# Kernel optimization log

Measured on AMD Instinct MI355X. Metric: run time of the kernel, lower is better.

The kernel has to match this reference:

```python
import jax, jax.numpy as jnp
import numpy as np

# Workspace layout (static slice bounds, per init_kwargs)
SS, SE = 0, 512        # spoke
HPS, HPE = 512, 768    # hub private
HSS, HSE = 768, 1024   # hub shared
TS, TE = 1024, 1088    # tag
HS, HE = 512, 1024     # full hub (priv + shared) for the read path

B, T, D_STATE, D_MODEL, D_LATENT = 8, 4096, 1088, 1024, 128


def setup_inputs() -> dict:
    key = jax.random.key(0)
    ks = jax.random.split(key, 10)
    scale = 0.02  # typical init scale for learned projections
    return {
        "S": jax.random.normal(ks[0], (B, T, D_STATE), jnp.float32),
        "w_spoke": jax.random.normal(ks[1], (B, T, SE - SS), jnp.float32),
        "w_hub_priv": jax.random.normal(ks[2], (B, T, HPE - HPS), jnp.float32),
        "w_hub_shared": jax.random.normal(ks[3], (B, T, HSE - HSS), jnp.float32),
        "tag": jax.random.normal(ks[4], (B, T, TE - TS), jnp.float32),
        "W_read": jax.random.normal(ks[5], (D_MODEL, D_STATE), jnp.float32) * scale,
        "cache": jnp.zeros((B, T, D_LATENT), jnp.float32),
        "latent": jax.random.normal(ks[6], (B, T, D_LATENT), jnp.float32),
        "Wk": jax.random.normal(ks[7], (D_MODEL, D_LATENT), jnp.float32) * scale,
        "Wv": jax.random.normal(ks[8], (D_MODEL, D_LATENT), jnp.float32) * scale,
    }


def reference(S, w_spoke, w_hub_priv, w_hub_shared, tag, W_read, cache, latent, Wk, Wv):
    # --- fused_workspace_write: four independent slice-adds into S ---
    S = S.at[:, :, SS:SE].add(w_spoke)
    S = S.at[:, :, HPS:HPE].add(w_hub_priv)
    S = S.at[:, :, HSS:HSE].add(w_hub_shared)
    S = S.at[:, :, TS:TE].add(tag)

    # --- fused_workspace_read: concat(spoke, hub, tag) then F.linear(., W_read) ---
    readable = jnp.concatenate(
        [S[:, :, SS:SE], S[:, :, HS:HE], S[:, :, TS:TE]], axis=-1
    )  # (B, T, D_STATE)
    out = jnp.einsum("btr,dr->btd", readable, W_read)  # (B, T, D_MODEL)

    # --- CWTLatentCache.update: overwrite latents at start_position=0 ---
    cache = jax.lax.dynamic_update_slice(cache, latent, (0, 0, 0))

    # --- K/V reconstruction from compressed latents via up-projections ---
    k = jnp.einsum("btl,dl->btd", cache, Wk)  # (B, T, D_MODEL)
    v = jnp.einsum("btl,dl->btd", cache, Wv)  # (B, T, D_MODEL)
    return (out, k, v)
```

## Files before the change

kernel.cpp:

```cpp
#include <hip/hip_runtime.h>

typedef __attribute__((ext_vector_type(8))) _Float16 half8;
typedef __attribute__((ext_vector_type(2))) __fp16 half2r;
typedef __attribute__((ext_vector_type(4))) float f32x4;

#define AS1 __attribute__((address_space(1)))
#define AS3 __attribute__((address_space(3)))

union H2U { half2r h; unsigned int u; };
union Frag { half8 v; unsigned long long d[2]; };

__device__ __forceinline__ unsigned int pk(float a, float b) {
    H2U x; x.h = __builtin_amdgcn_cvt_pkrtz(a, b); return x.u;
}

__device__ __forceinline__ void gload_lds16(const void* g, void* l) {
    __builtin_amdgcn_global_load_lds((const AS1 unsigned int*)g,
                                     (AS3 unsigned int*)l, 16, 0, 0);
}

#define W1_ROWB 2176
#define WS2_OFF 2228224
#define W2_ROWB 256
#define A_ROWB  2176

__device__ __forceinline__ void pick_w(int ks, const float* wsp, const float* whp,
                                       const float* whs, const float* wtg,
                                       const float*& wbase, int& wstr, int& wko) {
    if (ks < 8)       { wbase = wsp; wstr = 512; wko = ks * 64; }
    else if (ks < 12) { wbase = whp; wstr = 256; wko = ks * 64 - 512; }
    else if (ks < 16) { wbase = whs; wstr = 256; wko = ks * 64 - 768; }
    else              { wbase = wtg; wstr = 64;  wko = 0; }
}

__global__ __launch_bounds__(256) void prep_w(const float* __restrict__ Wr,
                                              const float* __restrict__ Wk,
                                              const float* __restrict__ Wv,
                                              char* __restrict__ ws) {
    int id = blockIdx.x * 256 + threadIdx.x;
    if (id < 272 * 1024) {
        int n = id / 272;
        int k = (id % 272) * 4;
        f32x4 w = *(const f32x4*)(Wr + (size_t)n * 1088 + k);
        uint2 q; q.x = pk(w.x, w.y); q.y = pk(w.z, w.w);
        size_t off = (size_t)n * W1_ROWB + ((k >> 6) << 7)
                   + (((k & 63) << 1) ^ ((n & 7) << 4));
        *(uint2*)(ws + off) = q;
    } else {
        int j = id - 272 * 1024;
        int r = j >> 5;
        int k = (j & 31) << 2;
        const float* src = (r < 1024) ? (Wk + (size_t)r * 128 + k)
                                      : (Wv + (size_t)(r - 1024) * 128 + k);
        f32x4 w = *(const f32x4*)src;
        uint2 q; q.x = pk(w.x, w.y); q.y = pk(w.z, w.w);
        size_t off = WS2_OFF + (size_t)r * W2_ROWB + ((k >> 6) << 7)
                   + (((k & 63) << 1) ^ ((r & 7) << 4));
        *(uint2*)(ws + off) = q;
    }
}

__global__ __launch_bounds__(256)
void fuse_a(const float* __restrict__ S, const float* __restrict__ wsp,
            const float* __restrict__ whp, const float* __restrict__ whs,
            const float* __restrict__ wtg, char* __restrict__ a16) {
    int u = blockIdx.x * 256 + threadIdx.x;
    int row = u / 272;
    int rem = u % 272;
    int ks = rem >> 4;
    int k4 = (rem & 15) << 2;

    const float* wbase; int wstr, wko;
    pick_w(ks, wsp, whp, whs, wtg, wbase, wstr, wko);

    f32x4 s4 = *(const f32x4*)(S + (size_t)row * 1088 + ks * 64 + k4);
    f32x4 w4 = *(const f32x4*)(wbase + (size_t)row * wstr + wko + k4);
    uint2 q; q.x = pk(s4.x + w4.x, s4.y + w4.y);
             q.y = pk(s4.z + w4.z, s4.w + w4.w);
    size_t off = (size_t)row * A_ROWB + (ks << 7)
               + (((k4) << 1) ^ ((row & 7) << 4));
    *(uint2*)(a16 + off) = q;
}

__global__ __launch_bounds__(256, 2)
void gemm_read(const char* __restrict__ wsA, const char* __restrict__ wws,
               float* __restrict__ out) {
    __shared__ char lds[65536];

    int bid = blockIdx.x;
    int wg   = (bid & 7) * 256 + (bid >> 3);
    int mblk = wg >> 3, nblk = wg & 7;
    int m0 = mblk << 7, n0 = nblk << 7;

    int tid = threadIdx.x;
    int lane = tid & 63, wid = tid >> 6;
    int wm = (wid >> 1) << 6, wn = (wid & 1) << 6;
    int lp = lane & 15, lg = lane >> 4;

    f32x4 acc[4][4] = {};

#define STAGE_T(KS, DL, BASE, ROWB, R0) do {                              \
        const char* grow = (BASE) + (size_t)(R0) * (ROWB) + (KS) * 128;   \
        _Pragma("unroll")                                                 \
        for (int c = 0; c < 4; ++c) {                                     \
            int s = c * 4096 + wid * 1024 + lane * 16;                    \
            int rr = s >> 7, cb = s & 127;                                \
            gload_lds16(grow + (size_t)rr * (ROWB) + cb,                  \
                        (DL) + c * 4096 + wid * 1024);                    \
        }                                                                 \
    } while (0)

#define COMPUTE(AL, BL) do {                                              \
        _Pragma("unroll")                                                 \
        for (int b = 0; b < 2; ++b) {                                     \
            Frag af[4], bf[4];                                            \
            _Pragma("unroll")                                             \
            for (int f = 0; f < 4; ++f) {                                 \
                int ra = wm + f * 16 + lp;  int xa = (ra & 7) << 4;       \
                af[f].d[0] = *(const unsigned long long*)((AL) + (ra << 7) + ((b * 64 + lg * 8) ^ xa));      \
                af[f].d[1] = *(const unsigned long long*)((AL) + (ra << 7) + ((b * 64 + 32 + lg * 8) ^ xa)); \
                int rb = wn + f * 16 + lp;  int xb = (rb & 7) << 4;       \
                bf[f].d[0] = *(const unsigned long long*)((BL) + (rb << 7) + ((b * 64 + lg * 8) ^ xb));      \
                bf[f].d[1] = *(const unsigned long long*)((BL) + (rb << 7) + ((b * 64 + 32 + lg * 8) ^ xb)); \
            }                                                             \
            _Pragma("unroll")                                             \
            for (int i = 0; i < 4; ++i)                                   \
                _Pragma("unroll")                                         \
                for (int j = 0; j < 4; ++j)                               \
                    acc[i][j] = __builtin_amdgcn_mfma_f32_16x16x32_f16(af[i].v, bf[j].v, acc[i][j], 0, 0, 0); \
        }                                                                 \
    } while (0)

    STAGE_T(0, lds,         wsA, A_ROWB,  m0);
    STAGE_T(0, lds + 32768, wws, W1_ROWB, n0);
    __syncthreads();

    for (int ks = 0; ks < 17; ++ks) {
        int co = (ks & 1) ? 16384 : 0;
        int no = co ^ 16384;
        if (ks < 16) {
            STAGE_T(ks + 1, lds + no,         wsA, A_ROWB,  m0);
            STAGE_T(ks + 1, lds + 32768 + no, wws, W1_ROWB, n0);
        }
        COMPUTE(lds + co, lds + 32768 + co);
        __syncthreads();
    }

    #pragma unroll
    for (int i = 0; i < 4; ++i)
        #pragma unroll
        for (int j = 0; j < 4; ++j) {
            int row = m0 + wm + i * 16 + (lg << 2);
            int col = n0 + wn + j * 16 + lp;
            float* p = out + (size_t)row * 1024 + col;
            #pragma unroll
            for (int r = 0; r < 4; ++r) p[(size_t)r * 1024] = acc[i][j][r];
        }
#undef STAGE_T
#undef COMPUTE
}

__global__ __launch_bounds__(256, 2)
void gemm_kv(const float* __restrict__ lat, const char* __restrict__ ws2,
             float* __restrict__ outk, float* __restrict__ outv) {
    __shared__ char lds[32768];
    char* Al = lds;
    char* Bl = lds + 16384;

    int bid = blockIdx.x;
    int wg   = (bid & 7) * 512 + (bid >> 3);
    int mblk = wg >> 4, nb = wg & 15;
    int m0 = mblk << 7;
    int nrow0 = nb << 7;
    float* out = (nb < 8) ? outk : outv;
    int n0 = (nb & 7) << 7;

    int tid = threadIdx.x;
    int lane = tid & 63, wid = tid >> 6;
    int wm = (wid >> 1) << 6, wn = (wid & 1) << 6;
    int lp = lane & 15, lg = lane >> 4;

    f32x4 acc[4][4] = {};

    for (int ks = 0; ks < 2; ++ks) {
        __syncthreads();
        {
            const char* wrow = ws2 + (size_t)nrow0 * W2_ROWB + ks * 128;
            #pragma unroll
            for (int c = 0; c < 4; ++c) {
                int s = c * 4096 + wid * 1024 + lane * 16;
                int n = s >> 7, cb = s & 127;
                gload_lds16(wrow + (size_t)n * W2_ROWB + cb,
                            Bl + c * 4096 + wid * 1024);
            }
        }
        #pragma unroll
        for (int i = 0; i < 8; ++i) {
            int u = i * 256 + tid;
            int row = u >> 4;
            int k4 = (u & 15) << 2;
            f32x4 s4 = *(const f32x4*)(lat + (size_t)(m0 + row) * 128 + ks * 64 + k4);
            uint2 q; q.x = pk(s4.x, s4.y); q.y = pk(s4.z, s4.w);
            *(uint2*)(Al + (row << 7) + ((k4 << 1) ^ ((row & 7) << 4))) = q;
        }
        __syncthreads();

        #pragma unroll
        for (int b = 0; b < 2; ++b) {
            Frag af[4], bf[4];
            #pragma unroll
            for (int f = 0; f < 4; ++f) {
                int ra = wm + f * 16 + lp;  int xa = (ra & 7) << 4;
                af[f].d[0] = *(const unsigned long long*)(Al + (ra << 7) + ((b * 64 + lg * 8) ^ xa));
                af[f].d[1] = *(const unsigned long long*)(Al + (ra << 7) + ((b * 64 + 32 + lg * 8) ^ xa));
                int rb = wn + f * 16 + lp;  int xb = (rb & 7) << 4;
                bf[f].d[0] = *(const unsigned long long*)(Bl + (rb << 7) + ((b * 64 + lg * 8) ^ xb));
                bf[f].d[1] = *(const unsigned long long*)(Bl + (rb << 7) + ((b * 64 + 32 + lg * 8) ^ xb));
            }
            #pragma unroll
            for (int i = 0; i < 4; ++i)
                #pragma unroll
                for (int j = 0; j < 4; ++j)
                    acc[i][j] = __builtin_amdgcn_mfma_f32_16x16x32_f16(af[i].v, bf[j].v, acc[i][j], 0, 0, 0);
        }
    }

    #pragma unroll
    for (int i = 0; i < 4; ++i)
        #pragma unroll
        for (int j = 0; j < 4; ++j) {
            int row = m0 + wm + i * 16 + (lg << 2);
            int col = n0 + wn + j * 16 + lp;
            float* p = out + (size_t)row * 1024 + col;
            #pragma unroll
            for (int r = 0; r < 4; ++r) p[(size_t)r * 1024] = acc[i][j][r];
        }
}

extern "C" void kernel_launch(void* const* d_in, const int* in_sizes, int n_in,
                              void* d_out, int out_size, void* d_ws, size_t ws_size,
                              hipStream_t stream) {
    const float* S   = (const float*)d_in[0];
    const float* wsp = (const float*)d_in[1];
    const float* whp = (const float*)d_in[2];
    const float* whs = (const float*)d_in[3];
    const float* wtg = (const float*)d_in[4];
    const float* Wr  = (const float*)d_in[5];
    const float* lat = (const float*)d_in[7];
    const float* Wk  = (const float*)d_in[8];
    const float* Wv  = (const float*)d_in[9];
    float* out = (float*)d_out;
    char*  ws  = (char*)d_ws;

    char* a16 = (char*)(out + 67108864ull);

    hipLaunchKernelGGL(prep_w, dim3(1344), dim3(256), 0, stream, Wr, Wk, Wv, ws);
    hipLaunchKernelGGL(fuse_a, dim3(34816), dim3(256), 0, stream,
                       S, wsp, whp, whs, wtg, a16);
    hipLaunchKernelGGL(gemm_read, dim3(2048), dim3(256), 0, stream,
                       a16, ws, out);
    hipLaunchKernelGGL(gemm_kv, dim3(4096), dim3(256), 0, stream,
                       lat, ws + WS2_OFF, out + 33554432ull, out + 67108864ull);
}
```

Before: 269.4 us.

## Deepen gemm_read to 256x128 tiles with triple-buffered LDS pipeline

The read GEMM now uses 512-thread blocks computing 256x128 output tiles, which halves the grid and reuses each B tile across twice as many rows. The LDS double buffer becomes a three-stage ring in dynamic shared memory, with vmcnt-based waits that keep two K-steps of loads in flight, and MFMA sections are wrapped in s_setprio. The aim is to hide global-to-LDS latency and cut B traffic. The cost is 144KB of LDS per block, which likely limits occupancy to one block per CU despite the launch bound requesting two.

```diff
diff --git a/kernel.cpp b/kernel.cpp
--- a/kernel.cpp
+++ b/kernel.cpp
@@ -23,6 +23,7 @@
 #define WS2_OFF 2228224
 #define W2_ROWB 256
 #define A_ROWB  2176
+#define TBUF    49152
 
 __device__ __forceinline__ void pick_w(int ks, const float* wsp, const float* whp,
                                        const float* whs, const float* wtg,
@@ -82,15 +83,15 @@
     *(uint2*)(a16 + off) = q;
 }
 
-__global__ __launch_bounds__(256, 2)
+__global__ __launch_bounds__(512, 2)
 void gemm_read(const char* __restrict__ wsA, const char* __restrict__ wws,
                float* __restrict__ out) {
-    __shared__ char lds[65536];
+    extern __shared__ char lds[];
 
     int bid = blockIdx.x;
-    int wg   = (bid & 7) * 256 + (bid >> 3);
+    int wg   = (bid & 7) * 128 + (bid >> 3);
     int mblk = wg >> 3, nblk = wg & 7;
-    int m0 = mblk << 7, n0 = nblk << 7;
+    int m0 = mblk << 8, n0 = nblk << 7;
 
     int tid = threadIdx.x;
     int lane = tid & 63, wid = tid >> 6;
@@ -99,51 +100,64 @@
 
     f32x4 acc[4][4] = {};
 
-#define STAGE_T(KS, DL, BASE, ROWB, R0) do {                              \
-        const char* grow = (BASE) + (size_t)(R0) * (ROWB) + (KS) * 128;   \
-        _Pragma("unroll")                                                 \
-        for (int c = 0; c < 4; ++c) {                                     \
-            int s = c * 4096 + wid * 1024 + lane * 16;                    \
-            int rr = s >> 7, cb = s & 127;                                \
-            gload_lds16(grow + (size_t)rr * (ROWB) + cb,                  \
-                        (DL) + c * 4096 + wid * 1024);                    \
-        }                                                                 \
+#define STAGE(T, DL) do {                                                  \
+        const char* garow = wsA + (size_t)m0 * A_ROWB + (size_t)(T) * 128; \
+        const char* gbrow = wws + (size_t)n0 * W1_ROWB + (size_t)(T) * 128;\
+        _Pragma("unroll")                                                  \
+        for (int c = 0; c < 4; ++c) {                                      \
+            int s = c * 8192 + wid * 1024 + lane * 16;                     \
+            gload_lds16(garow + (size_t)(s >> 7) * A_ROWB + (s & 127),     \
+                        (DL) + c * 8192 + wid * 1024);                     \
+        }                                                                  \
+        _Pragma("unroll")                                                  \
+        for (int c = 0; c < 2; ++c) {                                      \
+            int s = c * 8192 + wid * 1024 + lane * 16;                     \
+            gload_lds16(gbrow + (size_t)(s >> 7) * W1_ROWB + (s & 127),    \
+                        (DL) + 32768 + c * 8192 + wid * 1024);             \
+        }                                                                  \
     } while (0)
 
-#define COMPUTE(AL, BL) do {                                              \
-        _Pragma("unroll")                                                 \
-        for (int b = 0; b < 2; ++b) {                                     \
-            Frag af[4], bf[4];                                            \
-            _Pragma("unroll")                                             \
-            for (int f = 0; f < 4; ++f) {                                 \
-                int ra = wm + f * 16 + lp;  int xa = (ra & 7) << 4;       \
+#define COMPUTE(AL, BL) do {                                               \
+        _Pragma("unroll")                                                  \
+        for (int b = 0; b < 2; ++b) {                                      \
+            Frag af[4], bf[4];                                             \
+            _Pragma("unroll")                                              \
+            for (int f = 0; f < 4; ++f) {                                  \
+                int ra = wm + f * 16 + lp;  int xa = (ra & 7) << 4;        \
                 af[f].d[0] = *(const unsigned long long*)((AL) + (ra << 7) + ((b * 64 + lg * 8) ^ xa));      \
                 af[f].d[1] = *(const unsigned long long*)((AL) + (ra << 7) + ((b * 64 + 32 + lg * 8) ^ xa)); \
-                int rb = wn + f * 16 + lp;  int xb = (rb & 7) << 4;       \
+                int rb = wn + f * 16 + lp;  int xb = (rb & 7) << 4;        \
                 bf[f].d[0] = *(const unsigned long long*)((BL) + (rb << 7) + ((b * 64 + lg * 8) ^ xb));      \
                 bf[f].d[1] = *(const unsigned long long*)((BL) + (rb << 7) + ((b * 64 + 32 + lg * 8) ^ xb)); \
-            }                                                             \
-            _Pragma("unroll")                                             \
-            for (int i = 0; i < 4; ++i)                                   \
-                _Pragma("unroll")                                         \
-                for (int j = 0; j < 4; ++j)                               \
+            }                                                              \
+            __builtin_amdgcn_s_setprio(1);                                 \
+            _Pragma("unroll")                                              \
+            for (int i = 0; i < 4; ++i)                                    \
+                _Pragma("unroll")                                          \
+                for (int j = 0; j < 4; ++j)                                \
                     acc[i][j] = __builtin_amdgcn_mfma_f32_16x16x32_f16(af[i].v, bf[j].v, acc[i][j], 0, 0, 0); \
-        }                                                                 \
+            __builtin_amdgcn_s_setprio(0);                                 \
+        }                                                                  \
     } while (0)
 
-    STAGE_T(0, lds,         wsA, A_ROWB,  m0);
-    STAGE_T(0, lds + 32768, wws, W1_ROWB, n0);
-    __syncthreads();
-
-    for (int ks = 0; ks < 17; ++ks) {
-        int co = (ks & 1) ? 16384 : 0;
-        int no = co ^ 16384;
-        if (ks < 16) {
-            STAGE_T(ks + 1, lds + no,         wsA, A_ROWB,  m0);
-            STAGE_T(ks + 1, lds + 32768 + no, wws, W1_ROWB, n0);
-        }
-        COMPUTE(lds + co, lds + 32768 + co);
-        __syncthreads();
+    STAGE(0, lds);
+    STAGE(1, lds + TBUF);
+
+    for (int t = 0; t < 16; ++t) {
+        asm volatile("s_waitcnt vmcnt(6)" ::: "memory");
+        __builtin_amdgcn_s_barrier();
+        if (t < 15) {
+            char* nb = lds + ((t + 2) % 3) * TBUF;
+            STAGE(t + 2, nb);
+        }
+        const char* cb = lds + (t % 3) * TBUF;
+        COMPUTE(cb, cb + 32768);
+    }
+    asm volatile("s_waitcnt vmcnt(0)" ::: "memory");
+    __builtin_amdgcn_s_barrier();
+    {
+        const char* cb = lds + (16 % 3) * TBUF;
+        COMPUTE(cb, cb + 32768);
     }
 
     #pragma unroll
@@ -156,7 +170,7 @@
             #pragma unroll
             for (int r = 0; r < 4; ++r) p[(size_t)r * 1024] = acc[i][j][r];
         }
-#undef STAGE_T
+#undef STAGE
 #undef COMPUTE
 }
 
@@ -252,12 +266,19 @@
     float* out = (float*)d_out;
     char*  ws  = (char*)d_ws;
 
+    static bool lds_init = false;
+    if (!lds_init) {
+        hipFuncSetAttribute(reinterpret_cast<const void*>(gemm_read),
+                            hipFuncAttributeMaxDynamicSharedMemorySize, 3 * TBUF);
+        lds_init = true;
+    }
+
     char* a16 = (char*)(out + 67108864ull);
 
     hipLaunchKernelGGL(prep_w, dim3(1344), dim3(256), 0, stream, Wr, Wk, Wv, ws);
     hipLaunchKernelGGL(fuse_a, dim3(34816), dim3(256), 0, stream,
                        S, wsp, whp, whs, wtg, a16);
-    hipLaunchKernelGGL(gemm_read, dim3(2048), dim3(256), 0, stream,
+    hipLaunchKernelGGL(gemm_read, dim3(1024), dim3(512), 3 * TBUF, stream,
                        a16, ws, out);
     hipLaunchKernelGGL(gemm_kv, dim3(4096), dim3(256), 0, stream,
                        lat, ws + WS2_OFF, out + 33554432ull, out + 67108864ull);
```

After: 282.4 us. +4.8%, slower.
